# Optimization experiments

Measured on AMD Instinct MI355X. Metric: run time of the kernel, lower is better.

The kernel has to match this reference:

```python
import jax, jax.numpy as jnp
import numpy as np

BETA = 0.25  # commitment/codebook mixing as in VQVAE.__init__


def setup_inputs() -> dict:
    key = jax.random.key(0)
    k1, k2 = jax.random.split(key)
    # z: encoder latent [B, C, H, W] with C = latent_dim
    z = jax.random.normal(k1, (32, 64, 64, 64), dtype=jnp.float32)
    # codebook: nn.Embedding(num_embeddings, latent_dim).weight
    codebook = jax.random.normal(k2, (1024, 64), dtype=jnp.float32)
    return {"z": z, "codebook": codebook}


def reference(z, codebook):
    B, C, H, W = z.shape
    zf = z.reshape(B, C, H * W).transpose(0, 2, 1)  # [B, N, C], N = H*W
    # Squared Euclidean distances; argmin identical to torch.cdist(p=2) argmin
    # since sqrt is monotone (min_distances are unused in the original forward).
    d2 = (jnp.sum(zf * zf, axis=-1, keepdims=True)              # [B, N, 1]
          + jnp.sum(codebook * codebook, axis=-1)[None, None, :]  # [1, 1, K]
          - 2.0 * jnp.einsum('bnc,kc->bnk', zf, codebook))        # [B, N, K]
    indices = jnp.argmin(d2, axis=-1)                            # [B, N]
    z_q = codebook[indices]                                      # [B, N, C] gather
    z_q = z_q.transpose(0, 2, 1).reshape(B, C, H, W)
    commitment_loss = jnp.mean((jax.lax.stop_gradient(z_q) - z) ** 2)
    codebook_loss = jnp.mean((z_q - jax.lax.stop_gradient(z)) ** 2)
    loss = commitment_loss + BETA * codebook_loss
    return z_q, loss
```

## Files before the change

kernel.cpp:

```cpp
#include <hip/hip_runtime.h>
#include <float.h>

#define HW    4096
#define NC    64
#define NK    1024
#define NB    32
#define NPIX  (NB*HW)
#define TOTAL (NPIX*NC)
#define PPB   256

#define MARGIN 8e-3f

typedef __attribute__((ext_vector_type(8))) short short8;
typedef __attribute__((ext_vector_type(4))) float floatx4;

__device__ __forceinline__ unsigned short f2bf(float f) {
    unsigned u = __float_as_uint(f);
    u += 0x7FFFu + ((u >> 16) & 1u);
    return (unsigned short)(u >> 16);
}
__device__ __forceinline__ float bf2f(unsigned short h) {
    return __uint_as_float(((unsigned)h) << 16);
}

__global__ void vq_prep_kernel(const float* __restrict__ cb,
                               float* __restrict__ cnorm,
                               unsigned short* __restrict__ cb_hi,
                               unsigned short* __restrict__ cb_lo,
                               float* __restrict__ loss_out) {
    int k = blockIdx.x * 64 + threadIdx.x;
    if (k == 0) loss_out[0] = 0.0f;
    if (k < NK) {
        const float4* r4 = (const float4*)(cb + (size_t)k * NC);
        double s = 0.0;
        #pragma unroll
        for (int j = 0; j < 16; ++j) {
            float4 v = r4[j];
            const float fv[4] = {v.x, v.y, v.z, v.w};
            #pragma unroll
            for (int t = 0; t < 4; ++t) {
                float f = fv[t];
                unsigned short h = f2bf(f);
                unsigned short l = f2bf(f - bf2f(h));
                cb_hi[k * NC + 4 * j + t] = h;
                cb_lo[k * NC + 4 * j + t] = l;
                double dv = (double)f;
                s = fma(dv, dv, s);
            }
        }
        cnorm[k] = (float)s;
    }
}

__global__ __launch_bounds__(256, 2) void vq_mfma_kernel(
        const float* __restrict__ z,
        const float* __restrict__ cb,
        const unsigned short* __restrict__ cb_hi,
        const unsigned short* __restrict__ cb_lo,
        const float* __restrict__ cnorm,
        float* __restrict__ zq,
        float* __restrict__ loss_out) {
    __shared__ alignas(16) char smem[65536];
    __shared__ alignas(16) float cn_lds[NK];
    __shared__ int   finidx[PPB];
    __shared__ int   flags[PPB];
    __shared__ float redf[4];

    const int tid = threadIdx.x;
    const int g0  = blockIdx.x * PPB;
    const int bb  = g0 >> 12;
    const int pp0 = g0 & 4095;
    const float* zbase = z  + (size_t)bb * (NC * HW) + pp0;
    float*      zqbase = zq + (size_t)bb * (NC * HW) + pp0;

    ((float4*)cn_lds)[tid] = ((const float4*)cnorm)[tid];

    unsigned short (*zh)[PPB] = (unsigned short(*)[PPB])smem;
    unsigned short (*zl)[PPB] = (unsigned short(*)[PPB])(smem + 32768);
    {
        const int px4 = (tid & 63) * 4;
        const int c0  = tid >> 6;
        #pragma unroll
        for (int it = 0; it < 16; ++it) {
            const int c = it * 4 + c0;
            float4 v = *(const float4*)(zbase + (size_t)c * HW + px4);
            v.x *= -2.0f; v.y *= -2.0f; v.z *= -2.0f; v.w *= -2.0f;
            unsigned short h0 = f2bf(v.x), h1 = f2bf(v.y),
                           h2 = f2bf(v.z), h3 = f2bf(v.w);
            unsigned short l0 = f2bf(v.x - bf2f(h0)), l1 = f2bf(v.y - bf2f(h1)),
                           l2 = f2bf(v.z - bf2f(h2)), l3 = f2bf(v.w - bf2f(h3));
            uint2 ph = make_uint2((unsigned)h0 | ((unsigned)h1 << 16),
                                  (unsigned)h2 | ((unsigned)h3 << 16));
            uint2 pl = make_uint2((unsigned)l0 | ((unsigned)l1 << 16),
                                  (unsigned)l2 | ((unsigned)l3 << 16));
            *(uint2*)&zh[c][px4] = ph;
            *(uint2*)&zl[c][px4] = pl;
        }
    }
    __syncthreads();

    const int lane = tid & 63;
    const int w    = tid >> 6;
    const int q    = lane >> 4;
    const int pcol = lane & 15;

    short8 Bh0[4], Bh1[4], Bl0[4], Bl1[4];
    #pragma unroll
    for (int j = 0; j < 4; ++j) {
        const int px = w * 64 + j * 16 + pcol;
        #pragma unroll
        for (int t = 0; t < 8; ++t) {
            Bh0[j][t] = (short)zh[q * 8 + t][px];
            Bh1[j][t] = (short)zh[32 + q * 8 + t][px];
            Bl0[j][t] = (short)zl[q * 8 + t][px];
            Bl1[j][t] = (short)zl[32 + q * 8 + t][px];
        }
    }
    __syncthreads();

    uint4* abuf = (uint4*)smem;
    const int spart = tid >> 7;
    const int sidx  = tid & 127;
    const int srow  = sidx >> 3;
    const int schk  = sidx & 7;
    const int ldst  = spart * 128 + srow * 8 + (schk ^ (srow & 7));
    const char* gsrc = (spart == 0 ? (const char*)cb_hi : (const char*)cb_lo)
                       + (size_t)sidx * 16;

    const int ridx0 = pcol * 8 + (q ^ (pcol & 7));
    const int ridx1 = pcol * 8 + ((4 + q) ^ (pcol & 7));

    uint4 sreg = *(const uint4*)(gsrc);
    abuf[ldst] = sreg;
    sreg = *(const uint4*)(gsrc + 2048);
    __syncthreads();

    float B1[4] = {FLT_MAX, FLT_MAX, FLT_MAX, FLT_MAX};
    float B2[4] = {FLT_MAX, FLT_MAX, FLT_MAX, FLT_MAX};
    int   I1[4] = {0, 0, 0, 0};

    #pragma unroll 2
    for (int tile = 0; tile < 64; ++tile) {
        if (tile < 63) abuf[((tile + 1) & 1) * 256 + ldst] = sreg;
        if (tile < 62) sreg = *(const uint4*)(gsrc + (size_t)(tile + 2) * 2048);

        const short8* A = (const short8*)smem + (tile & 1) * 256;
        short8 ah0 = A[ridx0];
        short8 ah1 = A[ridx1];
        short8 al0 = A[128 + ridx0];
        short8 al1 = A[128 + ridx1];

        const floatx4 cn4 = *(const floatx4*)&cn_lds[tile * 16 + q * 4];
        const int kb = tile * 16 + q * 4;
        #pragma unroll
        for (int j = 0; j < 4; ++j) {
            floatx4 a0 = __builtin_amdgcn_mfma_f32_16x16x32_bf16(ah0, Bh0[j], cn4, 0, 0, 0);
            floatx4 a1 = {0.f, 0.f, 0.f, 0.f};
            a1 = __builtin_amdgcn_mfma_f32_16x16x32_bf16(ah1, Bh1[j], a1, 0, 0, 0);
            a0 = __builtin_amdgcn_mfma_f32_16x16x32_bf16(ah0, Bl0[j], a0, 0, 0, 0);
            a1 = __builtin_amdgcn_mfma_f32_16x16x32_bf16(ah1, Bl1[j], a1, 0, 0, 0);
            a0 = __builtin_amdgcn_mfma_f32_16x16x32_bf16(al0, Bh0[j], a0, 0, 0, 0);
            a1 = __builtin_amdgcn_mfma_f32_16x16x32_bf16(al1, Bh1[j], a1, 0, 0, 0);

            #pragma unroll
            for (int i = 0; i < 4; ++i) {
                float s = a0[i] + a1[i];
                bool lt = s < B1[j];
                I1[j] = lt ? (kb + i) : I1[j];
                B2[j] = __builtin_amdgcn_fmed3f(s, B1[j], B2[j]);
                B1[j] = fminf(s, B1[j]);
            }
        }
        __syncthreads();
    }

    #pragma unroll
    for (int j = 0; j < 4; ++j) {
        float b1 = B1[j], b2 = B2[j];
        int i1 = I1[j];
        #pragma unroll
        for (int d = 16; d <= 32; d <<= 1) {
            float ob1 = __shfl_xor(b1, d);
            float ob2 = __shfl_xor(b2, d);
            int   oi1 = __shfl_xor(i1, d);
            float nb2 = fminf(fmaxf(b1, ob1), fminf(b2, ob2));
            bool lt = (ob1 < b1) || (ob1 == b1 && oi1 < i1);
            b1 = lt ? ob1 : b1;
            i1 = lt ? oi1 : i1;
            b2 = nb2;
        }
        if (q == 0) {
            const int px = w * 64 + j * 16 + pcol;
            finidx[px] = i1;
            flags[px]  = (b2 - b1 < MARGIN) ? 1 : 0;
        }
    }
    int myflag = 0;
    __syncthreads();
    myflag = flags[tid];
    const int nflag = __syncthreads_count(myflag);

    if (nflag > 0) {
        double* red_s = reinterpret_cast<double*>(cn_lds);
        int*    red_i = reinterpret_cast<int*>(cn_lds + 512);
        for (int p = 0; p < PPB; ++p) {
            if (flags[p]) {
                const float* zp = zbase + p;
                double bd = 1.0e300; int bi = 0;
                #pragma unroll 1
                for (int r = 0; r < 4; ++r) {
                    const int k = tid * 4 + r;
                    const float* rowp = cb + (size_t)k * NC;
                    double s = 0.0;
                    for (int c = 0; c < NC; ++c) {
                        double t = (double)zp[(size_t)c * HW] - (double)rowp[c];
                        s = fma(t, t, s);
                    }
                    if (s < bd) { bd = s; bi = k; }
                }
                red_s[tid] = bd; red_i[tid] = bi;
                __syncthreads();
                if (tid < 64) {
                    double m = red_s[tid]; int mi = red_i[tid];
                    #pragma unroll
                    for (int t = 1; t < 4; ++t) {
                        double om = red_s[tid + 64 * t];
                        int    oi = red_i[tid + 64 * t];
                        if (om < m || (om == m && oi < mi)) { m = om; mi = oi; }
                    }
                    #pragma unroll
                    for (int off = 32; off > 0; off >>= 1) {
                        double om = __shfl_down(m, off);
                        int    oi = __shfl_down(mi, off);
                        if (om < m || (om == m && oi < mi)) { m = om; mi = oi; }
                    }
                    if (tid == 0) finidx[p] = mi;
                }
                __syncthreads();
            }
        }
        __syncthreads();
    }

    {
        const int p  = tid;
        const int fi = finidx[p];
        const float4* crow4 = (const float4*)(cb + (size_t)fi * NC);
        float sse = 0.f;
        #pragma unroll
        for (int j = 0; j < 16; ++j) {
            const float4 qv = crow4[j];
            const size_t c0 = (size_t)(4 * j) * HW + p;
            const float z0 = zbase[c0];
            const float z1 = zbase[c0 + HW];
            const float z2 = zbase[c0 + 2 * (size_t)HW];
            const float z3 = zbase[c0 + 3 * (size_t)HW];
            zqbase[c0]                  = qv.x;
            zqbase[c0 + HW]             = qv.y;
            zqbase[c0 + 2 * (size_t)HW] = qv.z;
            zqbase[c0 + 3 * (size_t)HW] = qv.w;
            float t0 = qv.x - z0, t1 = qv.y - z1, t2 = qv.z - z2, t3 = qv.w - z3;
            sse = fmaf(t0, t0, sse);
            sse = fmaf(t1, t1, sse);
            sse = fmaf(t2, t2, sse);
            sse = fmaf(t3, t3, sse);
        }
        #pragma unroll
        for (int off = 32; off > 0; off >>= 1) sse += __shfl_down(sse, off);
        if ((tid & 63) == 0) redf[tid >> 6] = sse;
        __syncthreads();
        if (tid == 0)
            atomicAdd(loss_out, (redf[0] + redf[1] + redf[2] + redf[3]) *
                                (1.25f / (float)TOTAL));
    }
}

extern "C" void kernel_launch(void* const* d_in, const int* in_sizes, int n_in,
                              void* d_out, int out_size, void* d_ws, size_t ws_size,
                              hipStream_t stream) {
    const float* z  = (const float*)d_in[0];
    const float* cb = (const float*)d_in[1];
    float* out      = (float*)d_out;
    float* zqp      = out;
    float* loss     = out + TOTAL;

    float* cnorm          = (float*)d_ws;
    unsigned short* cb_hi = (unsigned short*)((char*)d_ws + 4096);
    unsigned short* cb_lo = (unsigned short*)((char*)d_ws + 4096 + NK * NC * 2);

    vq_prep_kernel<<<16, 64, 0, stream>>>(cb, cnorm, cb_hi, cb_lo, loss);
    vq_mfma_kernel<<<NPIX / PPB, 256, 0, stream>>>(z, cb, cb_hi, cb_lo, cnorm,
                                                   zqp, loss);
}
```

Baseline: 184.3 us.

## Halve LDS staging to raise occupancy and parallelize codebook prep kernel

The z bf16 hi/lo staging buffer is cut from 64 KB to 32 KB by loading the two 32-channel halves in two passes, each followed by a register fetch. Launch bounds go from 2 to 4 blocks per SM so more blocks can be resident and hide latency. The prep kernel is also reworked to use 68 blocks of 256 threads, with vectorized bf16 split stores separated from the norm computation. In exchange the main kernel gains an extra sync pass, and the tighter register budget may cause spills given the 32 B-fragment registers plus the accumulators.

```diff
diff --git a/kernel.cpp b/kernel.cpp
--- a/kernel.cpp
+++ b/kernel.cpp
@@ -28,31 +28,38 @@
                                unsigned short* __restrict__ cb_hi,
                                unsigned short* __restrict__ cb_lo,
                                float* __restrict__ loss_out) {
-    int k = blockIdx.x * 64 + threadIdx.x;
-    if (k == 0) loss_out[0] = 0.0f;
-    if (k < NK) {
+    const int b = blockIdx.x;
+    if (b < 64) {
+        const int i = b * 256 + threadIdx.x;
+        if (i == 0) loss_out[0] = 0.0f;
+        float4 v = ((const float4*)cb)[i];
+        unsigned short h0 = f2bf(v.x), h1 = f2bf(v.y),
+                       h2 = f2bf(v.z), h3 = f2bf(v.w);
+        unsigned short l0 = f2bf(v.x - bf2f(h0)), l1 = f2bf(v.y - bf2f(h1)),
+                       l2 = f2bf(v.z - bf2f(h2)), l3 = f2bf(v.w - bf2f(h3));
+        uint2 ph = make_uint2((unsigned)h0 | ((unsigned)h1 << 16),
+                              (unsigned)h2 | ((unsigned)h3 << 16));
+        uint2 pl = make_uint2((unsigned)l0 | ((unsigned)l1 << 16),
+                              (unsigned)l2 | ((unsigned)l3 << 16));
+        ((uint2*)cb_hi)[i] = ph;
+        ((uint2*)cb_lo)[i] = pl;
+    } else {
+        const int k = (b - 64) * 256 + threadIdx.x;
         const float4* r4 = (const float4*)(cb + (size_t)k * NC);
         double s = 0.0;
         #pragma unroll
         for (int j = 0; j < 16; ++j) {
             float4 v = r4[j];
-            const float fv[4] = {v.x, v.y, v.z, v.w};
-            #pragma unroll
-            for (int t = 0; t < 4; ++t) {
-                float f = fv[t];
-                unsigned short h = f2bf(f);
-                unsigned short l = f2bf(f - bf2f(h));
-                cb_hi[k * NC + 4 * j + t] = h;
-                cb_lo[k * NC + 4 * j + t] = l;
-                double dv = (double)f;
-                s = fma(dv, dv, s);
-            }
+            s = fma((double)v.x, (double)v.x, s);
+            s = fma((double)v.y, (double)v.y, s);
+            s = fma((double)v.z, (double)v.z, s);
+            s = fma((double)v.w, (double)v.w, s);
         }
         cnorm[k] = (float)s;
     }
 }
 
-__global__ __launch_bounds__(256, 2) void vq_mfma_kernel(
+__global__ __launch_bounds__(256, 4) void vq_mfma_kernel(
         const float* __restrict__ z,
         const float* __restrict__ cb,
         const unsigned short* __restrict__ cb_hi,
@@ -60,7 +67,7 @@
         const float* __restrict__ cnorm,
         float* __restrict__ zq,
         float* __restrict__ loss_out) {
-    __shared__ alignas(16) char smem[65536];
+    __shared__ alignas(16) char smem[32768];
     __shared__ alignas(16) float cn_lds[NK];
     __shared__ int   finidx[PPB];
     __shared__ int   flags[PPB];
@@ -75,15 +82,23 @@
 
     ((float4*)cn_lds)[tid] = ((const float4*)cnorm)[tid];
 
+    const int lane = tid & 63;
+    const int w    = tid >> 6;
+    const int q    = lane >> 4;
+    const int pcol = lane & 15;
+
     unsigned short (*zh)[PPB] = (unsigned short(*)[PPB])smem;
-    unsigned short (*zl)[PPB] = (unsigned short(*)[PPB])(smem + 32768);
-    {
+    unsigned short (*zl)[PPB] = (unsigned short(*)[PPB])(smem + 16384);
+
+    short8 Bh[2][4], Bl[2][4];
+    #pragma unroll
+    for (int r = 0; r < 2; ++r) {
         const int px4 = (tid & 63) * 4;
         const int c0  = tid >> 6;
         #pragma unroll
-        for (int it = 0; it < 16; ++it) {
+        for (int it = 0; it < 8; ++it) {
             const int c = it * 4 + c0;
-            float4 v = *(const float4*)(zbase + (size_t)c * HW + px4);
+            float4 v = *(const float4*)(zbase + (size_t)(r * 32 + c) * HW + px4);
             v.x *= -2.0f; v.y *= -2.0f; v.z *= -2.0f; v.w *= -2.0f;
             unsigned short h0 = f2bf(v.x), h1 = f2bf(v.y),
                            h2 = f2bf(v.z), h3 = f2bf(v.w);
@@ -96,27 +111,18 @@
             *(uint2*)&zh[c][px4] = ph;
             *(uint2*)&zl[c][px4] = pl;
         }
-    }
-    __syncthreads();
-
-    const int lane = tid & 63;
-    const int w    = tid >> 6;
-    const int q    = lane >> 4;
-    const int pcol = lane & 15;
-
-    short8 Bh0[4], Bh1[4], Bl0[4], Bl1[4];
-    #pragma unroll
-    for (int j = 0; j < 4; ++j) {
-        const int px = w * 64 + j * 16 + pcol;
-        #pragma unroll
-        for (int t = 0; t < 8; ++t) {
-            Bh0[j][t] = (short)zh[q * 8 + t][px];
-            Bh1[j][t] = (short)zh[32 + q * 8 + t][px];
-            Bl0[j][t] = (short)zl[q * 8 + t][px];
-            Bl1[j][t] = (short)zl[32 + q * 8 + t][px];
-        }
-    }
-    __syncthreads();
+        __syncthreads();
+        #pragma unroll
+        for (int j = 0; j < 4; ++j) {
+            const int px = w * 64 + j * 16 + pcol;
+            #pragma unroll
+            for (int t = 0; t < 8; ++t) {
+                Bh[r][j][t] = (short)zh[q * 8 + t][px];
+                Bl[r][j][t] = (short)zl[q * 8 + t][px];
+            }
+        }
+        __syncthreads();
+    }
 
     uint4* abuf = (uint4*)smem;
     const int spart = tid >> 7;
@@ -154,13 +160,13 @@
         const int kb = tile * 16 + q * 4;
         #pragma unroll
         for (int j = 0; j < 4; ++j) {
-            floatx4 a0 = __builtin_amdgcn_mfma_f32_16x16x32_bf16(ah0, Bh0[j], cn4, 0, 0, 0);
+            floatx4 a0 = __builtin_amdgcn_mfma_f32_16x16x32_bf16(ah0, Bh[0][j], cn4, 0, 0, 0);
             floatx4 a1 = {0.f, 0.f, 0.f, 0.f};
-            a1 = __builtin_amdgcn_mfma_f32_16x16x32_bf16(ah1, Bh1[j], a1, 0, 0, 0);
-            a0 = __builtin_amdgcn_mfma_f32_16x16x32_bf16(ah0, Bl0[j], a0, 0, 0, 0);
-            a1 = __builtin_amdgcn_mfma_f32_16x16x32_bf16(ah1, Bl1[j], a1, 0, 0, 0);
-            a0 = __builtin_amdgcn_mfma_f32_16x16x32_bf16(al0, Bh0[j], a0, 0, 0, 0);
-            a1 = __builtin_amdgcn_mfma_f32_16x16x32_bf16(al1, Bh1[j], a1, 0, 0, 0);
+            a1 = __builtin_amdgcn_mfma_f32_16x16x32_bf16(ah1, Bh[1][j], a1, 0, 0, 0);
+            a0 = __builtin_amdgcn_mfma_f32_16x16x32_bf16(ah0, Bl[0][j], a0, 0, 0, 0);
+            a1 = __builtin_amdgcn_mfma_f32_16x16x32_bf16(ah1, Bl[1][j], a1, 0, 0, 0);
+            a0 = __builtin_amdgcn_mfma_f32_16x16x32_bf16(al0, Bh[0][j], a0, 0, 0, 0);
+            a1 = __builtin_amdgcn_mfma_f32_16x16x32_bf16(al1, Bh[1][j], a1, 0, 0, 0);
 
             #pragma unroll
             for (int i = 0; i < 4; ++i) {
@@ -288,7 +294,7 @@
     unsigned short* cb_hi = (unsigned short*)((char*)d_ws + 4096);
     unsigned short* cb_lo = (unsigned short*)((char*)d_ws + 4096 + NK * NC * 2);
 
-    vq_prep_kernel<<<16, 64, 0, stream>>>(cb, cnorm, cb_hi, cb_lo, loss);
+    vq_prep_kernel<<<68, 256, 0, stream>>>(cb, cnorm, cb_hi, cb_lo, loss);
     vq_mfma_kernel<<<NPIX / PPB, 256, 0, stream>>>(z, cb, cb_hi, cb_lo, cnorm,
                                                    zqp, loss);
 }
```

Measured after the change: 216.5 us. +17.5%, slower.
